# Kernel optimization log

Measured on AMD Instinct MI355X. Metric: run time of the kernel, lower is better.

The kernel has to match this reference:

```python
import jax, jax.numpy as jnp
import numpy as np
import math

MIN_NORM = 1e-15
EPS = 4e-3  # float32 boundary eps used by PoincareBall.proj
C = 1.0


def artanh(x):
    x = jnp.clip(x, -1.0 + 1e-7, 1.0 - 1e-7)
    return 0.5 * (jnp.log1p(x) - jnp.log1p(-x))


def _norm(x):
    return jnp.maximum(jnp.linalg.norm(x, axis=-1, keepdims=True), MIN_NORM)


def proj(x, c):
    n = _norm(x)
    maxnorm = (1.0 - EPS) / jnp.sqrt(c)
    return jnp.where(n > maxnorm, x / n * maxnorm, x)


def expmap0(u, c):
    sc = jnp.sqrt(c)
    n = _norm(u)
    return jnp.tanh(sc * n) * u / (sc * n)


def logmap0(p, c):
    sc = jnp.sqrt(c)
    n = _norm(p)
    return artanh(sc * n) * p / (sc * n)


def mobius_add(x, y, c):
    x2 = jnp.sum(x * x, -1, keepdims=True)
    y2 = jnp.sum(y * y, -1, keepdims=True)
    xy = jnp.sum(x * y, -1, keepdims=True)
    num = (1 + 2 * c * xy + c * y2) * x + (1 - c * x2) * y
    den = 1 + 2 * c * xy + c * c * x2 * y2
    return num / jnp.maximum(den, MIN_NORM)


def mobius_matvec(m, x, c):
    sc = jnp.sqrt(c)
    xn = _norm(x)
    mx = x @ m.T
    mxn = _norm(mx)
    res = jnp.tanh(mxn / xn * artanh(sc * xn)) * mx / (mxn * sc)
    zero = jnp.all(mx == 0, axis=-1, keepdims=True)
    return jnp.where(zero, jnp.zeros((), x.dtype), res)


def hnn_layer(x, W, b, c):
    # HypLinear (dropout=0, use_bias=1) followed by HypAct(relu); proj_tan0 is identity for PoincareBall.
    res = proj(mobius_matvec(W, x, c), c)
    hb = proj(expmap0(b.reshape(1, -1), c), c)
    res = proj(mobius_add(res, hb, c), c)
    xt = jax.nn.relu(logmap0(res, c))
    return proj(expmap0(xt, c), c)


def setup_inputs():
    key = jax.random.key(0)
    ks = jax.random.split(key, 5)
    B, N, K, D = 4, 2000, 5, 32
    H1, H2 = 160, 32  # H_layer1: 32 -> 32*5, H_layer2: 32 -> 32
    # points on the Poincare ball (small norm so logmap0 is well-conditioned)
    in_feats = 0.05 * jax.random.normal(ks[0], (B, N, D), jnp.float32)
    # one-hot neighbor adjacency [batch, agent, nei, agent]
    nei_idx = jax.random.randint(ks[1], (B, N, K), 0, N)
    in_nei = jax.nn.one_hot(nei_idx, N, dtype=jnp.float32)
    # xavier_uniform with gain sqrt(2), zero bias (reset_parameters)
    b1w = math.sqrt(2.0) * math.sqrt(6.0 / (H1 + D))
    b2w = math.sqrt(2.0) * math.sqrt(6.0 / (H2 + H2))
    W1 = jax.random.uniform(ks[2], (H1, D), jnp.float32, -b1w, b1w)
    W2 = jax.random.uniform(ks[3], (H2, H2), jnp.float32, -b2w, b2w)
    b1 = jnp.zeros((H1,), jnp.float32)
    b2 = jnp.zeros((H2,), jnp.float32)
    return {"in_feats": in_feats, "in_nei": in_nei, "W1": W1, "b1": b1,
            "W2": W2, "b2": b2, "h_dim": 32, "head": 5}


def reference(in_feats, in_nei, W1, b1, W2, b2, h_dim, head):
    c = C
    B, N, D = in_feats.shape
    K = in_nei.shape[2]
    # tangent-space features (proj_tan0 is identity)
    feats = logmap0(in_feats, c)                                   # [B,N,D]
    agent = proj(expmap0(feats[:, :, None, :], c), c)              # [B,N,1,D]
    # one-hot adjacency gather: equals matmul(in_nei, repeat(feats)) in the torch code
    nbr_t = jnp.einsum('bnkm,bmd->bnkd', in_nei, feats)            # [B,N,K,D]
    nbr = proj(expmap0(nbr_t, c), c)
    # query heads
    q = logmap0(hnn_layer(agent, W1, b1, c), c)                    # [B,N,1,h*head]
    q = q.reshape(B, N, 1, h_dim, head).transpose(0, 1, 4, 2, 3)   # [B,N,head,1,h]
    # key heads; the torch code recomputes H_layer1(neighbor_repr) for values with
    # identical weights/inputs (dropout=0), so values == keys and we reuse them.
    kv = logmap0(hnn_layer(nbr, W1, b1, c), c)
    kv = kv.reshape(B, N, K, h_dim, head).transpose(0, 1, 4, 2, 3)  # [B,N,head,K,h]
    att = jax.nn.softmax(jnp.einsum('bnhqd,bnhkd->bnhqk', q, kv), axis=-1)  # [B,N,head,1,K]
    att_record = att.reshape(B, N, head, K)
    out = jnp.einsum('bnhqk,bnhkd->bnhqd', att, kv).mean(axis=2)   # [B,N,1,h]
    out = out.reshape(B, N, h_dim)
    out = proj(expmap0(out, c), c)
    out = hnn_layer(out, W2, b2, c)                                # [B,N,32]
    return out, att_record
```

## Files before the change

kernel.cpp:

```cpp
#include <hip/hip_runtime.h>
#include <math.h>

#define BB 4
#define NN 2000
#define KK 5
#define DD 32
#define H1 160
#define HEAD 5
#define HDIM 32
#define MAXNORM 0.996f
#define MINN 1e-15f

#define NROWS (BB * NN * KK)
#define NF4   (NROWS * (NN / 4))
#define F4_PER_ROW (NN / 4)
#define G_BLOCKS 2000
#define SCAN_BLOCKS 9766
#define SCAN_STRIDE (SCAN_BLOCKS * 256)

typedef float vfloat4 __attribute__((ext_vector_type(4)));

__device__ __forceinline__ float artanh_f(float x) {
    x = fminf(fmaxf(x, -1.0f + 1e-7f), 1.0f - 1e-7f);
    return 0.5f * (log1pf(x) - log1pf(-x));
}

__device__ __forceinline__ float wave_sum(float v) {
#pragma unroll
    for (int o = 32; o > 0; o >>= 1) v += __shfl_xor(v, o, 64);
    return v;
}

__device__ __forceinline__ float wave_sum32(float v) {
#pragma unroll
    for (int o = 16; o > 0; o >>= 1) v += __shfl_xor(v, o, 64);
    return v;
}

__global__ __launch_bounds__(256) void scan_kernel(const float* __restrict__ nei,
                                                   int* __restrict__ idx) {
    unsigned t = blockIdx.x * 256u + threadIdx.x;
    const vfloat4* __restrict__ p = (const vfloat4*)nei;
    vfloat4 v[8];
#pragma unroll
    for (int j = 0; j < 8; ++j) {
        unsigned e = t + (unsigned)j * SCAN_STRIDE;
        if (e < NF4) v[j] = p[e];
    }
#pragma unroll
    for (int j = 0; j < 8; ++j) {
        unsigned e = t + (unsigned)j * SCAN_STRIDE;
        if (e < NF4) {
            int sub = -1;
            if (v[j][0] > 0.5f) sub = 0;
            if (v[j][1] > 0.5f) sub = 1;
            if (v[j][2] > 0.5f) sub = 2;
            if (v[j][3] > 0.5f) sub = 3;
            if (sub >= 0) {
                unsigned row = e / F4_PER_ROW;
                unsigned col = (e - row * F4_PER_ROW) * 4u + (unsigned)sub;
                idx[row] = (int)col;
            }
        }
    }
}

__global__ __launch_bounds__(256, 4) void g_kernel(const float* __restrict__ xin,
                                                   const float* __restrict__ W1,
                                                   const float* __restrict__ b1,
                                                   float* __restrict__ g) {
    int lane = threadIdx.x & 63;
    int wave = (int)blockIdx.x * 4 + (int)(threadIdx.x >> 6);
    bool j2ok = lane < (H1 - 128);

    float x = (lane < DD) ? xin[wave * DD + lane] : 0.f;

    float n = fmaxf(sqrtf(wave_sum(x * x)), MINN);
    float fa = artanh_f(n);
    float f = (fa / n) * x;
    float fn = fmaxf(fa, MINN);
    float tp = tanhf(fn);
    float p = (tp / fn) * f;
    float pn = tp;
    if (pn > MAXNORM) p *= MAXNORM / pn;
    float xn = fmaxf(fminf(pn, MAXNORM), MINN);

    float mx0 = 0.f, mx1 = 0.f, mx2 = 0.f;
#pragma unroll
    for (int d = 0; d < DD; ++d) {
        float pd = __shfl(p, d, 64);
        mx0 += W1[lane * DD + d] * pd;
        mx1 += W1[(lane + 64) * DD + d] * pd;
        if (j2ok) mx2 += W1[(lane + 128) * DD + d] * pd;
    }
    float m2 = mx0 * mx0 + mx1 * mx1 + (j2ok ? mx2 * mx2 : 0.f);
    float mxn = fmaxf(sqrtf(wave_sum(m2)), MINN);
    float tr = tanhf(mxn / xn * artanh_f(xn));
    float sc = tr / mxn;
    float r0 = sc * mx0, r1 = sc * mx1, r2 = sc * mx2;
    float rn = tr;
    if (rn > MAXNORM) { float s = MAXNORM / rn; r0 *= s; r1 *= s; r2 *= s; }
    rn = fminf(rn, MAXNORM);

    float bb0 = b1[lane], bb1 = b1[lane + 64], bb2 = j2ok ? b1[lane + 128] : 0.f;
    float bn = fmaxf(sqrtf(wave_sum(bb0 * bb0 + bb1 * bb1 + bb2 * bb2)), MINN);
    float tb = tanhf(bn);
    float bs = tb / bn;
    float h0 = bs * bb0, h1 = bs * bb1, h2 = bs * bb2;
    float hn = tb;
    if (hn > MAXNORM) { float s = MAXNORM / hn; h0 *= s; h1 *= s; h2 *= s; }
    hn = fminf(hn, MAXNORM);

    float x2s = rn * rn;
    float y2s = hn * hn;
    float xys = wave_sum(r0 * h0 + r1 * h1 + (j2ok ? r2 * h2 : 0.f));
    float ca = 1.f + 2.f * xys + y2s;
    float cb = 1.f - x2s;
    float den = fmaxf(1.f + 2.f * xys + x2s * y2s, MINN);
    float a0 = (ca * r0 + cb * h0) / den;
    float a1 = (ca * r1 + cb * h1) / den;
    float a2 = (ca * r2 + cb * h2) / den;
    float an = fmaxf(sqrtf(wave_sum(a0 * a0 + a1 * a1 + (j2ok ? a2 * a2 : 0.f))), MINN);
    if (an > MAXNORM) { float s = MAXNORM / an; a0 *= s; a1 *= s; a2 *= s; }
    float an2 = fmaxf(fminf(an, MAXNORM), MINN);

    float ls = artanh_f(an2) / an2;
    float t0 = fmaxf(ls * a0, 0.f), t1 = fmaxf(ls * a1, 0.f), t2 = fmaxf(ls * a2, 0.f);
    float tn = fmaxf(sqrtf(wave_sum(t0 * t0 + t1 * t1 + (j2ok ? t2 * t2 : 0.f))), MINN);
    float te = tanhf(tn);
    float es = te / tn;
    float y0 = es * t0, y1 = es * t1, y2 = es * t2;
    float yn = te;
    float s2 = (yn > MAXNORM) ? (MAXNORM / yn) : 1.f;
    y0 *= s2; y1 *= s2; y2 *= s2;
    float yn2 = fmaxf(fminf(yn, MAXNORM), MINN);
    float gs = artanh_f(yn2) / yn2;

    float* go = g + (size_t)wave * H1;
    go[lane] = gs * y0;
    go[lane + 64] = gs * y1;
    if (j2ok) go[lane + 128] = gs * y2;
}

__global__ __launch_bounds__(256, 4) void fused_att_out_kernel(const float* __restrict__ g,
                                                               const int* __restrict__ idx,
                                                               const float* __restrict__ W2,
                                                               const float* __restrict__ b2,
                                                               float* __restrict__ out,
                                                               float* __restrict__ att_out) {
    int wave = (blockIdx.x * blockDim.x + threadIdx.x) >> 6;
    int lane = threadIdx.x & 63;
    if (wave >= BB * NN) return;
    int r = wave;
    int b = r / NN;
    int d = lane & 31;

    const float* gq = g + (size_t)r * H1;
    float q[HEAD];
#pragma unroll
    for (int h = 0; h < HEAD; ++h) q[h] = gq[d * HEAD + h];

    int nb[KK];
#pragma unroll
    for (int k = 0; k < KK; ++k) nb[k] = idx[r * KK + k];
    float kv[KK][HEAD];
#pragma unroll
    for (int k = 0; k < KK; ++k) {
        const float* gk = g + (size_t)(b * NN + nb[k]) * H1 + d * HEAD;
#pragma unroll
        for (int h = 0; h < HEAD; ++h) kv[k][h] = gk[h];
    }
    float s[KK][HEAD];
#pragma unroll
    for (int k = 0; k < KK; ++k)
#pragma unroll
        for (int h = 0; h < HEAD; ++h) s[k][h] = wave_sum32(q[h] * kv[k][h]);

    float att[HEAD][KK];
#pragma unroll
    for (int h = 0; h < HEAD; ++h) {
        float mxv = s[0][h];
#pragma unroll
        for (int k = 1; k < KK; ++k) mxv = fmaxf(mxv, s[k][h]);
        float sum = 0.f;
#pragma unroll
        for (int k = 0; k < KK; ++k) { att[h][k] = expf(s[k][h] - mxv); sum += att[h][k]; }
        float inv = 1.f / sum;
#pragma unroll
        for (int k = 0; k < KK; ++k) att[h][k] *= inv;
    }
    if (lane < HEAD * KK) {
        int h = lane / KK, k = lane % KK;
        att_out[(size_t)r * HEAD * KK + lane] = att[h][k];
    }

    float o = 0.f;
#pragma unroll
    for (int h = 0; h < HEAD; ++h)
#pragma unroll
        for (int k = 0; k < KK; ++k) o += att[h][k] * kv[k][h];
    o *= (1.f / HEAD);

    float n = fmaxf(sqrtf(wave_sum32(o * o)), MINN);
    float to = tanhf(n);
    o *= to / n;
    float on = to;
    if (on > MAXNORM) o *= MAXNORM / on;
    float xn = fmaxf(fminf(on, MAXNORM), MINN);

    float mx = 0.f;
#pragma unroll
    for (int dd = 0; dd < HDIM; ++dd) {
        float od = __shfl(o, dd, 64);
        mx += W2[d * HDIM + dd] * od;
    }
    float mxn = fmaxf(sqrtf(wave_sum32(mx * mx)), MINN);
    float tr = tanhf(mxn / xn * artanh_f(xn));
    mx *= tr / mxn;
    float rn = tr;
    if (rn > MAXNORM) mx *= MAXNORM / rn;
    rn = fminf(rn, MAXNORM);

    float hb = b2[d];
    float bn = fmaxf(sqrtf(wave_sum32(hb * hb)), MINN);
    float tb = tanhf(bn);
    hb *= tb / bn;
    float hn = tb;
    if (hn > MAXNORM) hb *= MAXNORM / hn;
    hn = fminf(hn, MAXNORM);

    float x2s = rn * rn;
    float y2s = hn * hn;
    float xys = wave_sum32(mx * hb);
    float ca = 1.f + 2.f * xys + y2s;
    float cb = 1.f - x2s;
    float den = fmaxf(1.f + 2.f * xys + x2s * y2s, MINN);
    float a = (ca * mx + cb * hb) / den;
    float an = fmaxf(sqrtf(wave_sum32(a * a)), MINN);
    if (an > MAXNORM) a *= MAXNORM / an;
    float an2 = fmaxf(fminf(an, MAXNORM), MINN);

    a = fmaxf((artanh_f(an2) / an2) * a, 0.f);
    float tn = fmaxf(sqrtf(wave_sum32(a * a)), MINN);
    float te = tanhf(tn);
    a *= te / tn;
    float yn = te;
    if (yn > MAXNORM) a *= MAXNORM / yn;

    if (lane < HDIM) out[(size_t)r * HDIM + lane] = a;
}

extern "C" void kernel_launch(void* const* d_in, const int* in_sizes, int n_in,
                              void* d_out, int out_size, void* d_ws, size_t ws_size,
                              hipStream_t stream) {
    const float* in_feats = (const float*)d_in[0];
    const float* in_nei = (const float*)d_in[1];
    const float* W1 = (const float*)d_in[2];
    const float* b1 = (const float*)d_in[3];
    const float* W2 = (const float*)d_in[4];
    const float* b2 = (const float*)d_in[5];

    int* idx = (int*)d_ws;
    size_t idx_bytes = ((size_t)BB * NN * KK * sizeof(int) + 255) & ~(size_t)255;
    float* g = (float*)((char*)d_ws + idx_bytes);

    float* out = (float*)d_out;
    float* att = out + (size_t)BB * NN * HDIM;

    hipLaunchKernelGGL(g_kernel, dim3(G_BLOCKS), dim3(256), 0, stream,
                       in_feats, W1, b1, g);
    hipLaunchKernelGGL(scan_kernel, dim3(SCAN_BLOCKS), dim3(256), 0, stream,
                       in_nei, idx);
    hipLaunchKernelGGL(fused_att_out_kernel, dim3((BB * NN * 64 + 255) / 256), dim3(256), 0, stream,
                       g, idx, W2, b2, out, att);
}
```

Before: 544.9 us.

## Scan one-hot rows per wave with early exit after the first half

Rewrites the one-hot index scan so each wavefront owns one adjacency row. It loads the first 256 float4s with nontemporal loads and reads the rest of the row only if no hot element was found. The found position is reduced across the wave with a max shuffle. This is meant to skip roughly half of the large adjacency read on average. The cost is the extra ballot and shuffle plus branch divergence between waves.

```diff
diff --git a/kernel.cpp b/kernel.cpp
--- a/kernel.cpp
+++ b/kernel.cpp
@@ -12,11 +12,9 @@
 #define MINN 1e-15f
 
 #define NROWS (BB * NN * KK)
-#define NF4   (NROWS * (NN / 4))
 #define F4_PER_ROW (NN / 4)
 #define G_BLOCKS 2000
-#define SCAN_BLOCKS 9766
-#define SCAN_STRIDE (SCAN_BLOCKS * 256)
+#define SCAN_BLOCKS (NROWS / 4)
 
 typedef float vfloat4 __attribute__((ext_vector_type(4)));
 
@@ -39,30 +37,46 @@
 
 __global__ __launch_bounds__(256) void scan_kernel(const float* __restrict__ nei,
                                                    int* __restrict__ idx) {
-    unsigned t = blockIdx.x * 256u + threadIdx.x;
-    const vfloat4* __restrict__ p = (const vfloat4*)nei;
-    vfloat4 v[8];
-#pragma unroll
-    for (int j = 0; j < 8; ++j) {
-        unsigned e = t + (unsigned)j * SCAN_STRIDE;
-        if (e < NF4) v[j] = p[e];
-    }
-#pragma unroll
-    for (int j = 0; j < 8; ++j) {
-        unsigned e = t + (unsigned)j * SCAN_STRIDE;
-        if (e < NF4) {
-            int sub = -1;
-            if (v[j][0] > 0.5f) sub = 0;
-            if (v[j][1] > 0.5f) sub = 1;
-            if (v[j][2] > 0.5f) sub = 2;
-            if (v[j][3] > 0.5f) sub = 3;
-            if (sub >= 0) {
-                unsigned row = e / F4_PER_ROW;
-                unsigned col = (e - row * F4_PER_ROW) * 4u + (unsigned)sub;
-                idx[row] = (int)col;
+    int lane = threadIdx.x & 63;
+    int wave = (int)((blockIdx.x * 256u + threadIdx.x) >> 6);
+    const vfloat4* __restrict__ row = (const vfloat4*)(nei + (size_t)wave * NN);
+    int pos = -1;
+    vfloat4 v[4];
+
+#pragma unroll
+    for (int j = 0; j < 4; ++j)
+        v[j] = __builtin_nontemporal_load(row + (lane + 64 * j));
+#pragma unroll
+    for (int j = 0; j < 4; ++j) {
+        int base = (lane + 64 * j) * 4;
+        if (v[j][0] > 0.5f) pos = base;
+        if (v[j][1] > 0.5f) pos = base + 1;
+        if (v[j][2] > 0.5f) pos = base + 2;
+        if (v[j][3] > 0.5f) pos = base + 3;
+    }
+    if (__ballot(pos >= 0) == 0ull) {
+#pragma unroll
+        for (int j = 0; j < 4; ++j) {
+            int e = 256 + lane + 64 * j;
+            if (e < F4_PER_ROW) {
+                v[j] = __builtin_nontemporal_load(row + e);
+            } else {
+                vfloat4 z = {0.f, 0.f, 0.f, 0.f};
+                v[j] = z;
             }
         }
-    }
+#pragma unroll
+        for (int j = 0; j < 4; ++j) {
+            int base = (256 + lane + 64 * j) * 4;
+            if (v[j][0] > 0.5f) pos = base;
+            if (v[j][1] > 0.5f) pos = base + 1;
+            if (v[j][2] > 0.5f) pos = base + 2;
+            if (v[j][3] > 0.5f) pos = base + 3;
+        }
+    }
+#pragma unroll
+    for (int o = 32; o > 0; o >>= 1) pos = max(pos, __shfl_xor(pos, o, 64));
+    if (lane == 0) idx[wave] = pos;
 }
 
 __global__ __launch_bounds__(256, 4) void g_kernel(const float* __restrict__ xin,
```

Measured after the change: 504.8 us. 1.08x faster.
